# Kernel tuning notes

Hardware: AMD Instinct MI355X
Metric: run time of the kernel (lower is better)

Reference implementation:

```python
import jax, jax.numpy as jnp
import numpy as np

B, T, D = 4, 2048, 1024
H, DK = 8, 64
EPS = 1e-6

def _xavier(key, shape):
    fan_in, fan_out = shape[1], shape[0]
    lim = float(np.sqrt(6.0 / (fan_in + fan_out)))
    return jax.random.uniform(key, shape, jnp.float32, -lim, lim)

def setup_inputs() -> dict:
    key = jax.random.key(0)
    ks = jax.random.split(key, 7)
    x = jax.random.normal(ks[0], (B, T, D), jnp.float32)
    W_Q = _xavier(ks[1], (H * DK, D))
    W_K = _xavier(ks[2], (H * DK, D))
    W_V = _xavier(ks[3], (H * DK, D))
    W_g_w = _xavier(ks[4], (H * DK, D))
    W_g_b = jax.random.normal(ks[5], (H * DK,), jnp.float32) * 0.02
    W_O = _xavier(ks[6], (D, H * DK))
    decay_log = jnp.zeros((H,), jnp.float32)
    return {"x": x, "W_Q": W_Q, "W_K": W_K, "W_V": W_V,
            "W_g_w": W_g_w, "W_g_b": W_g_b, "W_O": W_O,
            "decay_log": decay_log}

def _phi(u):
    # ELU + 1 feature map (positive)
    return jax.nn.elu(u) + 1.0

def reference(x, W_Q, W_K, W_V, W_g_w, W_g_b, W_O, decay_log):
    b, t, d = x.shape
    q = _phi((x @ W_Q.T).reshape(b, t, H, DK))
    k = _phi((x @ W_K.T).reshape(b, t, H, DK))
    v = (x @ W_V.T).reshape(b, t, H, DK)
    gamma = jax.nn.sigmoid(decay_log)           # [H]
    g4 = gamma[None, :, None, None]             # [1,H,1,1]
    g3 = gamma[None, :, None]                   # [1,H,1]

    # time-major for scan: [T,B,H,DK]
    qT = jnp.moveaxis(q, 1, 0)
    kT = jnp.moveaxis(k, 1, 0)
    vT = jnp.moveaxis(v, 1, 0)

    S0 = jnp.zeros((b, H, DK, DK), x.dtype)
    z0 = jnp.zeros((b, H, DK), x.dtype)

    def step(carry, inp):
        S, z = carry
        qt, kt, vt = inp
        S = g4 * S + jnp.einsum('bhi,bhj->bhij', kt, vt)
        z = g3 * z + kt
        num = jnp.einsum('bhij,bhi->bhj', S, qt)
        den = jnp.sum(z * qt, axis=-1, keepdims=True) + EPS
        return (S, z), num / den

    _, ys = jax.lax.scan(step, (S0, z0), (qT, kT, vT))  # ys: [T,B,H,DK]
    outputs = jnp.moveaxis(ys, 0, 1)                    # [B,T,H,DK]

    gate = jax.nn.sigmoid(x @ W_g_w.T + W_g_b).reshape(b, t, H, DK)
    y = (outputs * gate).reshape(b, t, H * DK)
    return y @ W_O.T
```

## Files before the change

kernel.cpp:

```cpp
#include <hip/hip_runtime.h>
#include <cstdint>
#include <cstddef>

#define B_   4
#define T_   2048
#define D_   1024
#define H_   8
#define DK_  64
#define HD_  512
#define CH_  64
#define NC_  32
#define EPS_ 1e-6f

typedef __attribute__((ext_vector_type(4))) float f32x4;
typedef __attribute__((ext_vector_type(8))) short s16x8;

__device__ __forceinline__ unsigned short f2bf(float f) {
    unsigned int x = __float_as_uint(f);
    unsigned int r = (x + 0x7FFFu + ((x >> 16) & 1u)) >> 16;
    return (unsigned short)r;
}
__device__ __forceinline__ float bf2f(unsigned short u) {
    return __uint_as_float(((unsigned int)u) << 16);
}
__device__ __forceinline__ void ld4(const float* p, float* o) {
    float4 v = *(const float4*)p; o[0]=v.x; o[1]=v.y; o[2]=v.z; o[3]=v.w;
}
__device__ __forceinline__ void gl_lds16(const unsigned short* g, unsigned short* l) {
    __builtin_amdgcn_global_load_lds(
        (const __attribute__((address_space(1))) unsigned int*)g,
        (__attribute__((address_space(3))) unsigned int*)l, 16, 0, 0);
}

__global__ __launch_bounds__(256) void k_cvt_all(
    const float* __restrict__ x,
    const float* __restrict__ wq, const float* __restrict__ wk,
    const float* __restrict__ wv, const float* __restrict__ wgw,
    const float* __restrict__ wo,
    unsigned short* __restrict__ xb,
    unsigned short* __restrict__ wqb, unsigned short* __restrict__ wkb,
    unsigned short* __restrict__ wvb, unsigned short* __restrict__ wgb,
    unsigned short* __restrict__ wob)
{
    int bid = blockIdx.x;
    const float* src; unsigned short* dst; int idx;
    if (bid < 8192) {
        src = x; dst = xb; idx = bid * 256 + threadIdx.x;
    } else {
        int r = bid - 8192;
        int w = r >> 9;
        idx = (r & 511) * 256 + threadIdx.x;
        switch (w) {
            case 0:  src = wq;  dst = wqb; break;
            case 1:  src = wk;  dst = wkb; break;
            case 2:  src = wv;  dst = wvb; break;
            case 3:  src = wgw; dst = wgb; break;
            default: src = wo;  dst = wob; break;
        }
    }
    float4 v = ((const float4*)src)[idx];
    ushort4 o;
    o.x = f2bf(v.x); o.y = f2bf(v.y); o.z = f2bf(v.z); o.w = f2bf(v.w);
    ((ushort4*)dst)[idx] = o;
}

#define GT_M 128
#define GT_N 128
#define GBK  64
#define LDA  64

__global__ __launch_bounds__(256) void k_gemm_qkvg(
    const unsigned short* __restrict__ xb,
    const unsigned short* __restrict__ wqb, const unsigned short* __restrict__ wkb,
    const unsigned short* __restrict__ wvb, const unsigned short* __restrict__ wgb,
    const float* __restrict__ bias,
    unsigned short* __restrict__ qo, unsigned short* __restrict__ ko,
    unsigned short* __restrict__ vo, unsigned short* __restrict__ go)
{
    __shared__ unsigned short As[GT_M * LDA];
    __shared__ unsigned short Bs[GT_N * LDA];
    const int tid = threadIdx.x;
    const int id  = blockIdx.x;
    const int xcd = id & 7, per = id >> 3;
    const int mtile = xcd * 8 + (per & 7);
    const int combo = per >> 3;
    const int which = combo >> 2;
    const int nb    = combo & 3;
    const int m0    = mtile * GT_M;
    const int n0    = nb * GT_N;
    const unsigned short* Wp = (which == 0) ? wqb : (which == 1) ? wkb : (which == 2) ? wvb : wgb;
    unsigned short* Op       = (which == 0) ? qo  : (which == 1) ? ko  : (which == 2) ? vo  : go;
    const int K = D_;

    const int lane = tid & 63, wave = tid >> 6;
    const int wm = (wave >> 1) * 64, wn = (wave & 1) * 64;
    const int r16 = lane & 15, quad = lane >> 4;
    const int lrow = lane >> 3, lseg = lane & 7;
    const int sseg = lseg ^ lrow;
    const int rx   = r16 & 7;

    f32x4 acc[4][4];
    #pragma unroll
    for (int a = 0; a < 4; a++)
        #pragma unroll
        for (int b = 0; b < 4; b++) acc[a][b] = 0.0f;

    for (int ko_ = 0; ko_ < K; ko_ += GBK) {
        #pragma unroll
        for (int i = 0; i < 4; i++) {
            int chunk = wave * 4 + i;
            int row = chunk * 8 + lrow;
            gl_lds16(xb + (size_t)(m0 + row) * K + ko_ + sseg * 8, As + chunk * 512);
            gl_lds16(Wp + (size_t)(n0 + row) * K + ko_ + sseg * 8, Bs + chunk * 512);
        }
        __syncthreads();
        #pragma unroll
        for (int kk = 0; kk < GBK; kk += 32) {
            const int gb_ = kk >> 3;
            s16x8 af[4], bf[4];
            #pragma unroll
            for (int mt = 0; mt < 4; mt++)
                af[mt] = *(const s16x8*)&As[(wm + mt * 16 + r16) * LDA + (((gb_ + quad) ^ rx) << 3)];
            #pragma unroll
            for (int nt = 0; nt < 4; nt++)
                bf[nt] = *(const s16x8*)&Bs[(wn + nt * 16 + r16) * LDA + (((gb_ + quad) ^ rx) << 3)];
            #pragma unroll
            for (int mt = 0; mt < 4; mt++)
                #pragma unroll
                for (int nt = 0; nt < 4; nt++)
                    acc[mt][nt] = __builtin_amdgcn_mfma_f32_16x16x32_bf16(af[mt], bf[nt], acc[mt][nt], 0, 0, 0);
        }
        __syncthreads();
    }
    #pragma unroll
    for (int mt = 0; mt < 4; mt++) {
        #pragma unroll
        for (int nt = 0; nt < 4; nt++) {
            int col = n0 + wn + nt * 16 + r16;
            float bv = (which == 3) ? bias[col] : 0.0f;
            #pragma unroll
            for (int r = 0; r < 4; r++) {
                int row = m0 + wm + mt * 16 + quad * 4 + r;
                float v = acc[mt][nt][r];
                if (which <= 1)      v = (v > 0.0f) ? v + 1.0f : __builtin_expf(v);
                else if (which == 3) v = 1.0f / (1.0f + __builtin_expf(-(v + bv)));
                Op[(size_t)row * HD_ + col] = f2bf(v);
            }
        }
    }
}

__global__ __launch_bounds__(256) void k_gemm_out(
    const unsigned short* __restrict__ ogb, const unsigned short* __restrict__ wob,
    float* __restrict__ y)
{
    __shared__ unsigned short As[GT_M * LDA];
    __shared__ unsigned short Bs[GT_N * LDA];
    const int tid = threadIdx.x;
    const int id  = blockIdx.x;
    const int xcd = id & 7, per = id >> 3;
    const int m0 = (xcd * 8 + (per & 7)) * GT_M;
    const int n0 = (per >> 3) * GT_N;
    const int K = HD_;

    const int lane = tid & 63, wave = tid >> 6;
    const int wm = (wave >> 1) * 64, wn = (wave & 1) * 64;
    const int r16 = lane & 15, quad = lane >> 4;
    const int lrow = lane >> 3, lseg = lane & 7;
    const int sseg = lseg ^ lrow;
    const int rx   = r16 & 7;

    f32x4 acc[4][4];
    #pragma unroll
    for (int a = 0; a < 4; a++)
        #pragma unroll
        for (int b = 0; b < 4; b++) acc[a][b] = 0.0f;

    for (int ko_ = 0; ko_ < K; ko_ += GBK) {
        #pragma unroll
        for (int i = 0; i < 4; i++) {
            int chunk = wave * 4 + i;
            int row = chunk * 8 + lrow;
            gl_lds16(ogb + (size_t)(m0 + row) * K + ko_ + sseg * 8, As + chunk * 512);
            gl_lds16(wob + (size_t)(n0 + row) * K + ko_ + sseg * 8, Bs + chunk * 512);
        }
        __syncthreads();
        #pragma unroll
        for (int kk = 0; kk < GBK; kk += 32) {
            const int gb_ = kk >> 3;
            s16x8 af[4], bf[4];
            #pragma unroll
            for (int mt = 0; mt < 4; mt++)
                af[mt] = *(const s16x8*)&As[(wm + mt * 16 + r16) * LDA + (((gb_ + quad) ^ rx) << 3)];
            #pragma unroll
            for (int nt = 0; nt < 4; nt++)
                bf[nt] = *(const s16x8*)&Bs[(wn + nt * 16 + r16) * LDA + (((gb_ + quad) ^ rx) << 3)];
            #pragma unroll
            for (int mt = 0; mt < 4; mt++)
                #pragma unroll
                for (int nt = 0; nt < 4; nt++)
                    acc[mt][nt] = __builtin_amdgcn_mfma_f32_16x16x32_bf16(af[mt], bf[nt], acc[mt][nt], 0, 0, 0);
        }
        __syncthreads();
    }
    #pragma unroll
    for (int mt = 0; mt < 4; mt++)
        #pragma unroll
        for (int nt = 0; nt < 4; nt++) {
            int col = n0 + wn + nt * 16 + r16;
            #pragma unroll
            for (int r = 0; r < 4; r++) {
                int row = m0 + wm + mt * 16 + quad * 4 + r;
                y[(size_t)row * D_ + col] = acc[mt][nt][r];
            }
        }
}

__global__ __launch_bounds__(256) void k_chunk_sums(
    const unsigned short* __restrict__ Kb, const unsigned short* __restrict__ Vb,
    float* __restrict__ Ssum, float* __restrict__ zsum, const float* __restrict__ decay_log)
{
    __shared__ float kl[CH_ * 68];
    __shared__ float vl[CH_ * 68];
    const int tid = threadIdx.x;
    const int bc  = blockIdx.x;
    const int c   = bc & (NC_ - 1);
    const int bh  = bc >> 5;
    const int h   = bh & (H_ - 1);
    const int b   = bh >> 3;
    const float g  = 1.0f / (1.0f + __builtin_expf(-decay_log[h]));
    const float lg = __builtin_log2f(g);
    const int t0 = c * CH_;

    #pragma unroll
    for (int e = 0; e < 2; e++) {
        int lid = e * 256 + tid;
        int l = lid >> 3, d0 = (lid & 7) * 8;
        float w = __builtin_exp2f((float)(CH_ - 1 - l) * lg);
        size_t gidx = (size_t)(b * T_ + t0 + l) * HD_ + h * DK_ + d0;
        uint4 kraw = *(const uint4*)(Kb + gidx);
        uint4 vraw = *(const uint4*)(Vb + gidx);
        const unsigned short* kp = (const unsigned short*)&kraw;
        const unsigned short* vp = (const unsigned short*)&vraw;
        #pragma unroll
        for (int j = 0; j < 8; j++) {
            kl[l * 68 + d0 + j] = bf2f(kp[j]) * w;
            vl[l * 68 + d0 + j] = bf2f(vp[j]);
        }
    }
    __syncthreads();

    const int ti = tid >> 4, tj = tid & 15;
    const int i0 = ti * 4, j0 = tj * 4;
    float acc[4][4];
    #pragma unroll
    for (int r = 0; r < 4; r++)
        #pragma unroll
        for (int cc = 0; cc < 4; cc++) acc[r][cc] = 0.0f;

    for (int l = 0; l < CH_; l++) {
        float kv[4], vv[4];
        ld4(&kl[l * 68 + i0], kv);
        ld4(&vl[l * 68 + j0], vv);
        #pragma unroll
        for (int r = 0; r < 4; r++)
            #pragma unroll
            for (int cc = 0; cc < 4; cc++) acc[r][cc] += kv[r] * vv[cc];
    }
    size_t base = (size_t)bc * (DK_ * DK_);
    #pragma unroll
    for (int r = 0; r < 4; r++) {
        float4 st = make_float4(acc[r][0], acc[r][1], acc[r][2], acc[r][3]);
        *(float4*)&Ssum[base + (size_t)(i0 + r) * DK_ + j0] = st;
    }
    if (tid < DK_) {
        float s = 0.0f;
        for (int l = 0; l < CH_; l++) s += kl[l * 68 + tid];
        zsum[(size_t)bc * DK_ + tid] = s;
    }
}

__global__ __launch_bounds__(128) void k_chunk_scan(
    float* __restrict__ Ssum, float* __restrict__ zsum, const float* __restrict__ decay_log)
{
    const int tid = threadIdx.x;
    const int grp = blockIdx.x & 31;
    const int bh  = blockIdx.x >> 5;
    const int h   = bh & (H_ - 1);
    const float g  = 1.0f / (1.0f + __builtin_expf(-decay_log[h]));
    const float gC = __builtin_exp2f((float)CH_ * __builtin_log2f(g));
    int elem = grp * 128 + tid;
    float s = 0.0f;
    for (int c = 0; c < NC_; c++) {
        size_t idx = ((size_t)(bh * NC_ + c)) * 4096 + elem;
        float v = Ssum[idx];
        Ssum[idx] = s;
        s = gC * s + v;
    }
    if (grp == 0 && tid < DK_) {
        float z = 0.0f;
        for (int c = 0; c < NC_; c++) {
            size_t idx = ((size_t)(bh * NC_ + c)) * DK_ + tid;
            float v = zsum[idx];
            zsum[idx] = z;
            z = gC * z + v;
        }
    }
}

__global__ __launch_bounds__(256) void k_chunk_out(
    const unsigned short* __restrict__ Qb, const unsigned short* __restrict__ Kb,
    const unsigned short* __restrict__ Vb, const unsigned short* __restrict__ Gb,
    const float* __restrict__ Ssum, const float* __restrict__ zsum,
    unsigned short* __restrict__ OGb, const float* __restrict__ decay_log)
{
    __shared__ float BufA[CH_ * 68];
    __shared__ float BufB[CH_ * 68];
    __shared__ float BufC[CH_ * 68];
    __shared__ float den_l[CH_];
    __shared__ float zp_l[DK_];
    __shared__ float gpow[CH_ + 1];

    const int tid = threadIdx.x;
    const int bc  = blockIdx.x;
    const int c   = bc & (NC_ - 1);
    const int bh  = bc >> 5;
    const int h   = bh & (H_ - 1);
    const int b   = bh >> 3;
    const float g  = 1.0f / (1.0f + __builtin_expf(-decay_log[h]));
    const float lg = __builtin_log2f(g);
    const int t0 = c * CH_;

    if (tid <= CH_) gpow[tid] = __builtin_exp2f((float)tid * lg);
    if (tid < DK_)  zp_l[tid] = zsum[(size_t)bc * DK_ + tid];

    #pragma unroll
    for (int e = 0; e < 2; e++) {
        int lid = e * 256 + tid;
        int l = lid >> 3, d0 = (lid & 7) * 8;
        size_t gidx = (size_t)(b * T_ + t0 + l) * HD_ + h * DK_ + d0;
        uint4 qraw = *(const uint4*)(Qb + gidx);
        uint4 kraw = *(const uint4*)(Kb + gidx);
        const unsigned short* qp = (const unsigned short*)&qraw;
        const unsigned short* kp = (const unsigned short*)&kraw;
        #pragma unroll
        for (int j = 0; j < 8; j++) {
            BufA[(d0 + j) * 68 + l] = bf2f(qp[j]);
            BufB[(d0 + j) * 68 + l] = bf2f(kp[j]);
        }
    }
    {
        size_t base = (size_t)bc * 4096;
        #pragma unroll
        for (int e = 0; e < 4; e++) {
            int flat = (e * 256 + tid) * 4;
            int row = flat >> 6, c0 = flat & 63;
            *(float4*)&BufC[row * 68 + c0] = *(const float4*)&Ssum[base + flat];
        }
    }
    __syncthreads();

    const int ti = tid >> 4, tj = tid & 15;
    const int i0 = ti * 4, j0 = tj * 4;
    float sc[4][4], it[4][4];
    #pragma unroll
    for (int r = 0; r < 4; r++)
        #pragma unroll
        for (int cc = 0; cc < 4; cc++) { sc[r][cc] = 0.0f; it[r][cc] = 0.0f; }

    for (int d = 0; d < DK_; d++) {
        float qv[4], kv[4], sv[4];
        ld4(&BufA[d * 68 + i0], qv);
        ld4(&BufB[d * 68 + j0], kv);
        ld4(&BufC[d * 68 + j0], sv);
        #pragma unroll
        for (int r = 0; r < 4; r++)
            #pragma unroll
            for (int cc = 0; cc < 4; cc++) {
                sc[r][cc] += qv[r] * kv[cc];
                it[r][cc] += qv[r] * sv[cc];
            }
    }
    #pragma unroll
    for (int r = 0; r < 4; r++) {
        int i = i0 + r;
        #pragma unroll
        for (int cc = 0; cc < 4; cc++) {
            int jl = j0 + cc;
            sc[r][cc] = (jl <= i) ? sc[r][cc] * gpow[i - jl] : 0.0f;
            it[r][cc] *= gpow[i + 1];
        }
        float rs = sc[r][0] + sc[r][1] + sc[r][2] + sc[r][3];
        rs += __shfl_xor(rs, 1);
        rs += __shfl_xor(rs, 2);
        rs += __shfl_xor(rs, 4);
        rs += __shfl_xor(rs, 8);
        if (tj == 0) den_l[i] = rs;
    }
    __syncthreads();
    if (tid < DK_) {
        float dp = 0.0f;
        for (int d = 0; d < DK_; d++) dp += BufA[d * 68 + tid] * zp_l[d];
        den_l[tid] += gpow[tid + 1] * dp + EPS_;
    }
    __syncthreads();
    #pragma unroll
    for (int cc = 0; cc < 4; cc++) {
        float4 st = make_float4(sc[0][cc], sc[1][cc], sc[2][cc], sc[3][cc]);
        *(float4*)&BufA[(j0 + cc) * 68 + i0] = st;
    }
    #pragma unroll
    for (int e = 0; e < 2; e++) {
        int lid = e * 256 + tid;
        int l = lid >> 3, d0 = (lid & 7) * 8;
        size_t gidx = (size_t)(b * T_ + t0 + l) * HD_ + h * DK_ + d0;
        uint4 vraw = *(const uint4*)(Vb + gidx);
        const unsigned short* vp = (const unsigned short*)&vraw;
        #pragma unroll
        for (int j = 0; j < 8; j++) BufB[l * 68 + d0 + j] = bf2f(vp[j]);
    }
    __syncthreads();

    float og[4][4];
    #pragma unroll
    for (int r = 0; r < 4; r++)
        #pragma unroll
        for (int cc = 0; cc < 4; cc++) og[r][cc] = it[r][cc];

    for (int jl = 0; jl < CH_; jl++) {
        float scv[4], vv[4];
        ld4(&BufA[jl * 68 + i0], scv);
        ld4(&BufB[jl * 68 + j0], vv);
        #pragma unroll
        for (int r = 0; r < 4; r++)
            #pragma unroll
            for (int cc = 0; cc < 4; cc++) og[r][cc] += scv[r] * vv[cc];
    }
    #pragma unroll
    for (int r = 0; r < 4; r++) {
        int i = i0 + r;
        float rcp = 1.0f / den_l[i];
        size_t gidx = (size_t)(b * T_ + t0 + i) * HD_ + h * DK_ + j0;
        ushort4 graw = *(const ushort4*)(Gb + gidx);
        ushort4 o;
        o.x = f2bf(og[r][0] * rcp * bf2f(graw.x));
        o.y = f2bf(og[r][1] * rcp * bf2f(graw.y));
        o.z = f2bf(og[r][2] * rcp * bf2f(graw.z));
        o.w = f2bf(og[r][3] * rcp * bf2f(graw.w));
        *(ushort4*)(OGb + gidx) = o;
    }
}

extern "C" void kernel_launch(void* const* d_in, const int* in_sizes, int n_in,
                              void* d_out, int out_size, void* d_ws, size_t ws_size,
                              hipStream_t stream)
{
    (void)in_sizes; (void)n_in; (void)out_size; (void)ws_size;
    const float* x         = (const float*)d_in[0];
    const float* W_Q       = (const float*)d_in[1];
    const float* W_K       = (const float*)d_in[2];
    const float* W_V       = (const float*)d_in[3];
    const float* W_gw      = (const float*)d_in[4];
    const float* W_gb      = (const float*)d_in[5];
    const float* W_O       = (const float*)d_in[6];
    const float* decay_log = (const float*)d_in[7];
    float* y = (float*)d_out;

    char* ws = (char*)d_ws;
    size_t off = 0;
    auto alloc = [&](size_t bytes) { void* p = ws + off; off += (bytes + 255) & ~(size_t)255; return p; };
    unsigned short* xb   = (unsigned short*)alloc((size_t)B_ * T_ * D_ * 2);
    unsigned short* wqb  = (unsigned short*)alloc((size_t)HD_ * D_ * 2);
    unsigned short* wkb  = (unsigned short*)alloc((size_t)HD_ * D_ * 2);
    unsigned short* wvb  = (unsigned short*)alloc((size_t)HD_ * D_ * 2);
    unsigned short* wgb  = (unsigned short*)alloc((size_t)HD_ * D_ * 2);
    unsigned short* wob  = (unsigned short*)alloc((size_t)D_ * HD_ * 2);
    unsigned short* qb   = (unsigned short*)alloc((size_t)B_ * T_ * HD_ * 2);
    unsigned short* kb   = (unsigned short*)alloc((size_t)B_ * T_ * HD_ * 2);
    unsigned short* vb   = (unsigned short*)alloc((size_t)B_ * T_ * HD_ * 2);
    unsigned short* gb   = (unsigned short*)alloc((size_t)B_ * T_ * HD_ * 2);
    unsigned short* ogb  = (unsigned short*)alloc((size_t)B_ * T_ * HD_ * 2);
    float* Ssum = (float*)alloc((size_t)B_ * H_ * NC_ * DK_ * DK_ * 4);
    float* zsum = (float*)alloc((size_t)B_ * H_ * NC_ * DK_ * 4);

    k_cvt_all<<<8192 + 5 * 512, 256, 0, stream>>>(x, W_Q, W_K, W_V, W_gw, W_O,
                                                  xb, wqb, wkb, wvb, wgb, wob);
    k_gemm_qkvg<<<1024, 256, 0, stream>>>(xb, wqb, wkb, wvb, wgb, W_gb, qb, kb, vb, gb);
    k_chunk_sums<<<B_ * H_ * NC_, 256, 0, stream>>>(kb, vb, Ssum, zsum, decay_log);
    k_chunk_scan<<<B_ * H_ * NC_, 128, 0, stream>>>(Ssum, zsum, decay_log);
    k_chunk_out<<<B_ * H_ * NC_, 256, 0, stream>>>(qb, kb, vb, gb, Ssum, zsum, ogb, decay_log);
    k_gemm_out<<<512, 256, 0, stream>>>(ogb, wob, y);
}
```

Baseline: 220.6 us.

## Double-buffer LDS tiles in projection GEMMs to overlap loads with MFMA

Both the QKVG projection GEMM and the output GEMM now use two LDS buffers per operand. The next K-tile is issued into the alternate buffer right after the loop-top barrier, so global-to-LDS loads can overlap the MFMA work on the current tile. This doubles shared memory per block, which may reduce occupancy. An unused srow variable is left in the code.

New measurement: 217.6 us. No clear change (-1.3%).

```diff
diff --git a/kernel.cpp b/kernel.cpp
--- a/kernel.cpp
+++ b/kernel.cpp
@@ -77,8 +77,8 @@
     unsigned short* __restrict__ qo, unsigned short* __restrict__ ko,
     unsigned short* __restrict__ vo, unsigned short* __restrict__ go)
 {
-    __shared__ unsigned short As[GT_M * LDA];
-    __shared__ unsigned short Bs[GT_N * LDA];
+    __shared__ unsigned short As[2][GT_M * LDA];
+    __shared__ unsigned short Bs[2][GT_N * LDA];
     const int tid = threadIdx.x;
     const int id  = blockIdx.x;
     const int xcd = id & 7, per = id >> 3;
@@ -91,6 +91,7 @@
     const unsigned short* Wp = (which == 0) ? wqb : (which == 1) ? wkb : (which == 2) ? wvb : wgb;
     unsigned short* Op       = (which == 0) ? qo  : (which == 1) ? ko  : (which == 2) ? vo  : go;
     const int K = D_;
+    const int NIT = K / GBK;
 
     const int lane = tid & 63, wave = tid >> 6;
     const int wm = (wave >> 1) * 64, wn = (wave & 1) * 64;
@@ -105,25 +106,33 @@
         #pragma unroll
         for (int b = 0; b < 4; b++) acc[a][b] = 0.0f;
 
-    for (int ko_ = 0; ko_ < K; ko_ += GBK) {
+    const int srow = wave * 32 + lrow * 4;
+
+    auto stage = [&](int buf, int ko_) {
         #pragma unroll
         for (int i = 0; i < 4; i++) {
             int chunk = wave * 4 + i;
             int row = chunk * 8 + lrow;
-            gl_lds16(xb + (size_t)(m0 + row) * K + ko_ + sseg * 8, As + chunk * 512);
-            gl_lds16(Wp + (size_t)(n0 + row) * K + ko_ + sseg * 8, Bs + chunk * 512);
-        }
+            gl_lds16(xb + (size_t)(m0 + row) * K + ko_ + sseg * 8, &As[buf][chunk * 512]);
+            gl_lds16(Wp + (size_t)(n0 + row) * K + ko_ + sseg * 8, &Bs[buf][chunk * 512]);
+        }
+    };
+
+    stage(0, 0);
+    for (int it = 0; it < NIT; ++it) {
         __syncthreads();
+        if (it + 1 < NIT) stage((it + 1) & 1, (it + 1) * GBK);
+        const int buf = it & 1;
         #pragma unroll
         for (int kk = 0; kk < GBK; kk += 32) {
             const int gb_ = kk >> 3;
             s16x8 af[4], bf[4];
             #pragma unroll
             for (int mt = 0; mt < 4; mt++)
-                af[mt] = *(const s16x8*)&As[(wm + mt * 16 + r16) * LDA + (((gb_ + quad) ^ rx) << 3)];
+                af[mt] = *(const s16x8*)&As[buf][(wm + mt * 16 + r16) * LDA + (((gb_ + quad) ^ rx) << 3)];
             #pragma unroll
             for (int nt = 0; nt < 4; nt++)
-                bf[nt] = *(const s16x8*)&Bs[(wn + nt * 16 + r16) * LDA + (((gb_ + quad) ^ rx) << 3)];
+                bf[nt] = *(const s16x8*)&Bs[buf][(wn + nt * 16 + r16) * LDA + (((gb_ + quad) ^ rx) << 3)];
             #pragma unroll
             for (int mt = 0; mt < 4; mt++)
                 #pragma unroll
@@ -132,6 +141,7 @@
         }
         __syncthreads();
     }
+    (void)srow;
     #pragma unroll
     for (int mt = 0; mt < 4; mt++) {
         #pragma unroll
@@ -154,14 +164,15 @@
     const unsigned short* __restrict__ ogb, const unsigned short* __restrict__ wob,
     float* __restrict__ y)
 {
-    __shared__ unsigned short As[GT_M * LDA];
-    __shared__ unsigned short Bs[GT_N * LDA];
+    __shared__ unsigned short As[2][GT_M * LDA];
+    __shared__ unsigned short Bs[2][GT_N * LDA];
     const int tid = threadIdx.x;
     const int id  = blockIdx.x;
     const int xcd = id & 7, per = id >> 3;
     const int m0 = (xcd * 8 + (per & 7)) * GT_M;
     const int n0 = (per >> 3) * GT_N;
     const int K = HD_;
+    const int NIT = K / GBK;
 
     const int lane = tid & 63, wave = tid >> 6;
     const int wm = (wave >> 1) * 64, wn = (wave & 1) * 64;
@@ -176,25 +187,31 @@
         #pragma unroll
         for (int b = 0; b < 4; b++) acc[a][b] = 0.0f;
 
-    for (int ko_ = 0; ko_ < K; ko_ += GBK) {
+    auto stage = [&](int buf, int ko_) {
         #pragma unroll
         for (int i = 0; i < 4; i++) {
             int chunk = wave * 4 + i;
             int row = chunk * 8 + lrow;
-            gl_lds16(ogb + (size_t)(m0 + row) * K + ko_ + sseg * 8, As + chunk * 512);
-            gl_lds16(wob + (size_t)(n0 + row) * K + ko_ + sseg * 8, Bs + chunk * 512);
-        }
+            gl_lds16(ogb + (size_t)(m0 + row) * K + ko_ + sseg * 8, &As[buf][chunk * 512]);
+            gl_lds16(wob + (size_t)(n0 + row) * K + ko_ + sseg * 8, &Bs[buf][chunk * 512]);
+        }
+    };
+
+    stage(0, 0);
+    for (int it = 0; it < NIT; ++it) {
         __syncthreads();
+        if (it + 1 < NIT) stage((it + 1) & 1, (it + 1) * GBK);
+        const int buf = it & 1;
         #pragma unroll
         for (int kk = 0; kk < GBK; kk += 32) {
             const int gb_ = kk >> 3;
             s16x8 af[4], bf[4];
             #pragma unroll
             for (int mt = 0; mt < 4; mt++)
-                af[mt] = *(const s16x8*)&As[(wm + mt * 16 + r16) * LDA + (((gb_ + quad) ^ rx) << 3)];
+                af[mt] = *(const s16x8*)&As[buf][(wm + mt * 16 + r16) * LDA + (((gb_ + quad) ^ rx) << 3)];
             #pragma unroll
             for (int nt = 0; nt < 4; nt++)
-                bf[nt] = *(const s16x8*)&Bs[(wn + nt * 16 + r16) * LDA + (((gb_ + quad) ^ rx) << 3)];
+                bf[nt] = *(const s16x8*)&Bs[buf][(wn + nt * 16 + r16) * LDA + (((gb_ + quad) ^ rx) << 3)];
             #pragma unroll
             for (int mt = 0; mt < 4; mt++)
                 #pragma unroll
```

## Fuse inter-chunk state scan into chunk_out and enlarge QKVG GEMM M-tile

Applied to the files above, without the earlier changes.

Removes the separate k_chunk_scan kernel. Each chunk_out block now recomputes its own prefix state by looping over all previous chunks' Ssum/zsum with decay gC. This saves a launch and a read-modify-write pass, but adds redundant, unbalanced reads: later chunks read up to 31 states each, roughly quadratic traffic. The QKVG GEMM also switches to 256x128 tiles with 8x4 MFMA accumulators per wave and half the blocks. This improves operand reuse at the cost of more registers and LDS.

Result: slower. 246.1 us (+11.6%).

```diff
diff --git a/kernel.cpp b/kernel.cpp
--- a/kernel.cpp
+++ b/kernel.cpp
@@ -64,12 +64,10 @@
     ((ushort4*)dst)[idx] = o;
 }
 
-#define GT_M 128
-#define GT_N 128
 #define GBK  64
 #define LDA  64
 
-__global__ __launch_bounds__(256) void k_gemm_qkvg(
+__global__ __launch_bounds__(256, 2) void k_gemm_qkvg(
     const unsigned short* __restrict__ xb,
     const unsigned short* __restrict__ wqb, const unsigned short* __restrict__ wkb,
     const unsigned short* __restrict__ wvb, const unsigned short* __restrict__ wgb,
@@ -77,55 +75,63 @@
     unsigned short* __restrict__ qo, unsigned short* __restrict__ ko,
     unsigned short* __restrict__ vo, unsigned short* __restrict__ go)
 {
-    __shared__ unsigned short As[GT_M * LDA];
-    __shared__ unsigned short Bs[GT_N * LDA];
+    __shared__ unsigned short As[256 * LDA];
+    __shared__ unsigned short Bs[128 * LDA];
     const int tid = threadIdx.x;
     const int id  = blockIdx.x;
     const int xcd = id & 7, per = id >> 3;
-    const int mtile = xcd * 8 + (per & 7);
-    const int combo = per >> 3;
+    const int mtile = xcd * 4 + (per & 3);
+    const int combo = per >> 2;
     const int which = combo >> 2;
     const int nb    = combo & 3;
-    const int m0    = mtile * GT_M;
-    const int n0    = nb * GT_N;
+    const int m0    = mtile * 256;
+    const int n0    = nb * 128;
     const unsigned short* Wp = (which == 0) ? wqb : (which == 1) ? wkb : (which == 2) ? wvb : wgb;
     unsigned short* Op       = (which == 0) ? qo  : (which == 1) ? ko  : (which == 2) ? vo  : go;
     const int K = D_;
+    const int NIT = K / GBK;
 
     const int lane = tid & 63, wave = tid >> 6;
-    const int wm = (wave >> 1) * 64, wn = (wave & 1) * 64;
+    const int wm = (wave >> 1) * 128, wn = (wave & 1) * 64;
     const int r16 = lane & 15, quad = lane >> 4;
     const int lrow = lane >> 3, lseg = lane & 7;
     const int sseg = lseg ^ lrow;
     const int rx   = r16 & 7;
 
-    f32x4 acc[4][4];
-    #pragma unroll
-    for (int a = 0; a < 4; a++)
+    f32x4 acc[8][4];
+    #pragma unroll
+    for (int a = 0; a < 8; a++)
         #pragma unroll
         for (int b = 0; b < 4; b++) acc[a][b] = 0.0f;
 
-    for (int ko_ = 0; ko_ < K; ko_ += GBK) {
+    for (int it = 0; it < NIT; ++it) {
+        const int ko_ = it * GBK;
+        #pragma unroll
+        for (int i = 0; i < 8; i++) {
+            int chunk = wave * 8 + i;
+            int row = chunk * 8 + lrow;
+            gl_lds16(xb + (size_t)(m0 + row) * K + ko_ + sseg * 8, As + chunk * 512);
+        }
         #pragma unroll
         for (int i = 0; i < 4; i++) {
             int chunk = wave * 4 + i;
             int row = chunk * 8 + lrow;
-            gl_lds16(xb + (size_t)(m0 + row) * K + ko_ + sseg * 8, As + chunk * 512);
             gl_lds16(Wp + (size_t)(n0 + row) * K + ko_ + sseg * 8, Bs + chunk * 512);
         }
         __syncthreads();
         #pragma unroll
         for (int kk = 0; kk < GBK; kk += 32) {
             const int gb_ = kk >> 3;
-            s16x8 af[4], bf[4];
-            #pragma unroll
-            for (int mt = 0; mt < 4; mt++)
-                af[mt] = *(const s16x8*)&As[(wm + mt * 16 + r16) * LDA + (((gb_ + quad) ^ rx) << 3)];
+            const int goff = (((gb_ + quad) ^ rx) << 3);
+            s16x8 af[8], bf[4];
+            #pragma unroll
+            for (int mt = 0; mt < 8; mt++)
+                af[mt] = *(const s16x8*)&As[(wm + mt * 16 + r16) * LDA + goff];
             #pragma unroll
             for (int nt = 0; nt < 4; nt++)
-                bf[nt] = *(const s16x8*)&Bs[(wn + nt * 16 + r16) * LDA + (((gb_ + quad) ^ rx) << 3)];
-            #pragma unroll
-            for (int mt = 0; mt < 4; mt++)
+                bf[nt] = *(const s16x8*)&Bs[(wn + nt * 16 + r16) * LDA + goff];
+            #pragma unroll
+            for (int mt = 0; mt < 8; mt++)
                 #pragma unroll
                 for (int nt = 0; nt < 4; nt++)
                     acc[mt][nt] = __builtin_amdgcn_mfma_f32_16x16x32_bf16(af[mt], bf[nt], acc[mt][nt], 0, 0, 0);
@@ -133,7 +139,7 @@
         __syncthreads();
     }
     #pragma unroll
-    for (int mt = 0; mt < 4; mt++) {
+    for (int mt = 0; mt < 8; mt++) {
         #pragma unroll
         for (int nt = 0; nt < 4; nt++) {
             int col = n0 + wn + nt * 16 + r16;
@@ -154,13 +160,13 @@
     const unsigned short* __restrict__ ogb, const unsigned short* __restrict__ wob,
     float* __restrict__ y)
 {
-    __shared__ unsigned short As[GT_M * LDA];
-    __shared__ unsigned short Bs[GT_N * LDA];
+    __shared__ unsigned short As[128 * LDA];
+    __shared__ unsigned short Bs[128 * LDA];
     const int tid = threadIdx.x;
     const int id  = blockIdx.x;
     const int xcd = id & 7, per = id >> 3;
-    const int m0 = (xcd * 8 + (per & 7)) * GT_M;
-    const int n0 = (per >> 3) * GT_N;
+    const int m0 = (xcd * 8 + (per & 7)) * 128;
+    const int n0 = (per >> 3) * 128;
     const int K = HD_;
 
     const int lane = tid & 63, wave = tid >> 6;
@@ -188,13 +194,14 @@
         #pragma unroll
         for (int kk = 0; kk < GBK; kk += 32) {
             const int gb_ = kk >> 3;
+            const int goff = (((gb_ + quad) ^ rx) << 3);
             s16x8 af[4], bf[4];
             #pragma unroll
             for (int mt = 0; mt < 4; mt++)
-                af[mt] = *(const s16x8*)&As[(wm + mt * 16 + r16) * LDA + (((gb_ + quad) ^ rx) << 3)];
+                af[mt] = *(const s16x8*)&As[(wm + mt * 16 + r16) * LDA + goff];
             #pragma unroll
             for (int nt = 0; nt < 4; nt++)
-                bf[nt] = *(const s16x8*)&Bs[(wn + nt * 16 + r16) * LDA + (((gb_ + quad) ^ rx) << 3)];
+                bf[nt] = *(const s16x8*)&Bs[(wn + nt * 16 + r16) * LDA + goff];
             #pragma unroll
             for (int mt = 0; mt < 4; mt++)
                 #pragma unroll
@@ -280,34 +287,6 @@
     }
 }
 
-__global__ __launch_bounds__(128) void k_chunk_scan(
-    float* __restrict__ Ssum, float* __restrict__ zsum, const float* __restrict__ decay_log)
-{
-    const int tid = threadIdx.x;
-    const int grp = blockIdx.x & 31;
-    const int bh  = blockIdx.x >> 5;
-    const int h   = bh & (H_ - 1);
-    const float g  = 1.0f / (1.0f + __builtin_expf(-decay_log[h]));
-    const float gC = __builtin_exp2f((float)CH_ * __builtin_log2f(g));
-    int elem = grp * 128 + tid;
-    float s = 0.0f;
-    for (int c = 0; c < NC_; c++) {
-        size_t idx = ((size_t)(bh * NC_ + c)) * 4096 + elem;
-        float v = Ssum[idx];
-        Ssum[idx] = s;
-        s = gC * s + v;
-    }
-    if (grp == 0 && tid < DK_) {
-        float z = 0.0f;
-        for (int c = 0; c < NC_; c++) {
-            size_t idx = ((size_t)(bh * NC_ + c)) * DK_ + tid;
-            float v = zsum[idx];
-            zsum[idx] = z;
-            z = gC * z + v;
-        }
-    }
-}
-
 __global__ __launch_bounds__(256) void k_chunk_out(
     const unsigned short* __restrict__ Qb, const unsigned short* __restrict__ Kb,
     const unsigned short* __restrict__ Vb, const unsigned short* __restrict__ Gb,
@@ -329,10 +308,35 @@
     const int b   = bh >> 3;
     const float g  = 1.0f / (1.0f + __builtin_expf(-decay_log[h]));
     const float lg = __builtin_log2f(g);
+    const float gC = __builtin_exp2f((float)CH_ * lg);
     const int t0 = c * CH_;
 
     if (tid <= CH_) gpow[tid] = __builtin_exp2f((float)tid * lg);
-    if (tid < DK_)  zp_l[tid] = zsum[(size_t)bc * DK_ + tid];
+
+    {
+        f32x4 sp[4];
+        #pragma unroll
+        for (int q = 0; q < 4; q++) sp[q] = 0.0f;
+        const int flat = tid * 16;
+        for (int cp = 0; cp < c; cp++) {
+            const float* src = Ssum + (size_t)(bh * NC_ + cp) * 4096 + flat;
+            #pragma unroll
+            for (int q = 0; q < 4; q++) {
+                f32x4 v = *(const f32x4*)(src + q * 4);
+                sp[q] = sp[q] * gC + v;
+            }
+        }
+        int row = tid >> 2, col0 = (tid & 3) * 16;
+        #pragma unroll
+        for (int q = 0; q < 4; q++)
+            *(f32x4*)&BufC[row * 68 + col0 + q * 4] = sp[q];
+    }
+    if (tid < DK_) {
+        float zp = 0.0f;
+        for (int cp = 0; cp < c; cp++)
+            zp = zp * gC + zsum[(size_t)(bh * NC_ + cp) * DK_ + tid];
+        zp_l[tid] = zp;
+    }
 
     #pragma unroll
     for (int e = 0; e < 2; e++) {
@@ -347,15 +351,6 @@
         for (int j = 0; j < 8; j++) {
             BufA[(d0 + j) * 68 + l] = bf2f(qp[j]);
             BufB[(d0 + j) * 68 + l] = bf2f(kp[j]);
-        }
-    }
-    {
-        size_t base = (size_t)bc * 4096;
-        #pragma unroll
-        for (int e = 0; e < 4; e++) {
-            int flat = (e * 256 + tid) * 4;
-            int row = flat >> 6, c0 = flat & 63;
-            *(float4*)&BufC[row * 68 + c0] = *(const float4*)&Ssum[base + flat];
         }
     }
     __syncthreads();
@@ -485,9 +480,8 @@
 
     k_cvt_all<<<8192 + 5 * 512, 256, 0, stream>>>(x, W_Q, W_K, W_V, W_gw, W_O,
                                                   xb, wqb, wkb, wvb, wgb, wob);
-    k_gemm_qkvg<<<1024, 256, 0, stream>>>(xb, wqb, wkb, wvb, wgb, W_gb, qb, kb, vb, gb);
+    k_gemm_qkvg<<<512, 256, 0, stream>>>(xb, wqb, wkb, wvb, wgb, W_gb, qb, kb, vb, gb);
     k_chunk_sums<<<B_ * H_ * NC_, 256, 0, stream>>>(kb, vb, Ssum, zsum, decay_log);
-    k_chunk_scan<<<B_ * H_ * NC_, 128, 0, stream>>>(Ssum, zsum, decay_log);
     k_chunk_out<<<B_ * H_ * NC_, 256, 0, stream>>>(qb, kb, vb, gb, Ssum, zsum, ogb, decay_log);
     k_gemm_out<<<512, 256, 0, stream>>>(ogb, wob, y);
 }
```
